# Optimization experiments

Measured on AMD Instinct MI355X. Metric: run time of the kernel, lower is better.

## Reference

```python
import jax, jax.numpy as jnp
import numpy as np
import math

S = 3  # num_subset

def _pe(C, T, V, domain):
    # sinusoidal positional encoding over flattened (T,V) grid -> [1,C,T,V]
    if domain == 'spatial':
        pos = np.tile(np.arange(V), T).astype(np.float32)
    else:
        pos = np.repeat(np.arange(T), V).astype(np.float32)
    div = np.exp(np.arange(0, C, 2).astype(np.float32) * (-math.log(10000.0) / C))
    pe = np.zeros((T * V, C), np.float32)
    pe[:, 0::2] = np.sin(pos[:, None] * div)
    pe[:, 1::2] = np.cos(pos[:, None] * div)
    return jnp.asarray(pe.reshape(T, V, C).transpose(2, 0, 1)[None])

def _conv1(x, W, b):  # 1x1 Conv2d == per-pixel channel matmul
    return jnp.einsum('oc,nctv->notv', W, x) + b[None, :, None, None]

def _bn(x, p):  # eval-mode BatchNorm2d; p: [4,C] = gamma, beta, run_mean, run_var
    g, b, m, v = p
    inv = g / jnp.sqrt(v + 1e-5)
    return (x - m[:, None, None]) * inv[:, None, None] + b[:, None, None]

def _lrelu(x):
    return jnp.where(x > 0, x, 0.1 * x)  # LeakyReLU(0.1)

def _forward(x, Wqk_s, bqk_s, alphas, att0s, Wo_s, bo_s, bn_o_s, Wf_s, bf_s, bn_f_s,
             Wqk_t, bqk_t, alphat, att0t, Wo_t, bo_t, bn_o_t, Wf_t, bf_t, bn_f_t):
    N, C, T, V = x.shape
    R = Wqk_s.shape[0] // (2 * S)  # inter_channels
    # ---- spatial attention (atts buffer is zeros; downs are identity since in==out, stride=1) ----
    y = x + _pe(C, T, V, 'spatial')
    qk = _conv1(y, Wqk_s, bqk_s).reshape(N, 2 * S, R, T, V)
    q, k = qk[:, :S], qk[:, S:]
    att = jnp.tanh(jnp.einsum('nsctu,nsctv->nsuv', q, k) / (R * T)) * alphas + att0s
    y = jnp.einsum('nctu,nsuv->nsctv', x, att).reshape(N, S * C, T, V)
    y = _lrelu(x + _bn(_conv1(y, Wo_s, bo_s), bn_o_s))      # out_nets + residual
    y = _lrelu(x + _bn(_conv1(y, Wf_s, bf_s), bn_f_s))      # ff_nets  + residual
    # ---- temporal attention (attt buffer is zeros; downt are identity) ----
    z = y + _pe(C, T, V, 'temporal')
    qk = _conv1(z, Wqk_t, bqk_t).reshape(N, 2 * S, R, T, V)
    q, k = qk[:, :S], qk[:, S:]
    att = jnp.tanh(jnp.einsum('nsctv,nscqv->nstq', q, k) / (R * V)) * alphat + att0t
    z = jnp.einsum('nctv,nstq->nscqv', y, att).reshape(N, S * C, T, V)
    z = _lrelu(y + _bn(_conv1(z, Wo_t, bo_t), bn_o_t))      # out_nett + residual
    z = _lrelu(y + _bn(_conv1(z, Wf_t, bf_t), bn_f_t))      # ff_nett  + residual
    return z

def setup_inputs() -> dict:
    key = jax.random.key(0)
    ks = jax.random.split(key, 12)
    N, C, T, V, R = 128, 128, 64, 25, 32
    def w(k, o, i):
        return jax.random.normal(k, (o, i), jnp.float32) * np.float32(np.sqrt(2.0 / i))
    def bnp(k, c):
        k1, k2, k3 = jax.random.split(k, 3)
        return jnp.stack([1.0 + 0.1 * jax.random.normal(k1, (c,)),
                          0.1 * jax.random.normal(k2, (c,)),
                          0.1 * jax.random.normal(k3, (c,)),
                          jnp.ones((c,))])
    return {
        'x': jax.random.normal(ks[0], (N, C, T, V), jnp.float32),
        'Wqk_s': w(ks[1], 2 * S * R, C), 'bqk_s': jnp.zeros((2 * S * R,), jnp.float32),
        'alphas': jnp.ones((1, S, 1, 1), jnp.float32),
        'att0s': jnp.ones((1, S, V, V), jnp.float32) / V,
        'Wo_s': w(ks[2], C, S * C), 'bo_s': jnp.zeros((C,), jnp.float32), 'bn_o_s': bnp(ks[3], C),
        'Wf_s': w(ks[4], C, C), 'bf_s': jnp.zeros((C,), jnp.float32), 'bn_f_s': bnp(ks[5], C),
        'Wqk_t': w(ks[6], 2 * S * R, C), 'bqk_t': jnp.zeros((2 * S * R,), jnp.float32),
        'alphat': jnp.ones((1, S, 1, 1), jnp.float32),
        'att0t': jnp.broadcast_to(jnp.eye(T, dtype=jnp.float32), (1, S, T, T)).copy(),
        'Wo_t': w(ks[7], C, S * C), 'bo_t': jnp.zeros((C,), jnp.float32), 'bn_o_t': bnp(ks[8], C),
        'Wf_t': w(ks[9], C, C), 'bf_t': jnp.zeros((C,), jnp.float32), 'bn_f_t': bnp(ks[10], C),
    }

def reference(x, Wqk_s, bqk_s, alphas, att0s, Wo_s, bo_s, bn_o_s, Wf_s, bf_s, bn_f_s,
              Wqk_t, bqk_t, alphat, att0t, Wo_t, bo_t, bn_o_t, Wf_t, bf_t, bn_f_t):
    return _forward(x, Wqk_s, bqk_s, alphas, att0s, Wo_s, bo_s, bn_o_s, Wf_s, bf_s, bn_f_s,
                    Wqk_t, bqk_t, alphat, att0t, Wo_t, bo_t, bn_o_t, Wf_t, bf_t, bn_f_t)
```

## Files before the change

kernel.cpp:

```cpp
#include <hip/hip_runtime.h>
#include <math.h>


typedef __attribute__((ext_vector_type(8))) short short8v;
typedef __attribute__((ext_vector_type(4))) float f32x4;

__device__ __forceinline__ ushort f2bf(float f) {
    uint b = __float_as_uint(f);
    uint r = b + 0x7fffu + ((b >> 16) & 1u);
    return (ushort)(r >> 16);
}
__device__ __forceinline__ float bf2f(ushort h) {
    return __uint_as_float(((uint)h) << 16);
}

__global__ __launch_bounds__(256) void wt_prep(
    const float* __restrict__ Wo_s, const float* __restrict__ Wf_s,
    const float* __restrict__ Wo_t, const float* __restrict__ Wf_t,
    const float* __restrict__ Wqk_s, const float* __restrict__ Wqk_t,
    ushort* __restrict__ W16)
{
    int idx = blockIdx.x * 256 + threadIdx.x;
    if (idx >= 180224) return;
    float v;
    if (idx < 49152) {
        int s = idx / 16384, rem = idx % 16384, o = rem / 128, c = rem % 128;
        v = Wo_s[o * 384 + s * 128 + c];
    } else if (idx < 65536) {
        v = Wf_s[idx - 49152];
    } else if (idx < 114688) {
        int i = idx - 65536, s = i / 16384, rem = i % 16384, o = rem / 128, c = rem % 128;
        v = Wo_t[o * 384 + s * 128 + c];
    } else if (idx < 131072) {
        v = Wf_t[idx - 114688];
    } else if (idx < 155648) {
        v = Wqk_s[idx - 131072];
    } else {
        v = Wqk_t[idx - 155648];
    }
    W16[idx] = f2bf(v);
}

__global__ __launch_bounds__(256) void qk_pe_mfma(
    const float* __restrict__ src, const ushort* __restrict__ Wbf,
    const float* __restrict__ bias, ushort* __restrict__ out, int pos_is_t)
{
    __shared__ __align__(16) ushort xT[160 * 136];
    __shared__ __align__(16) ushort exch[192 * 24];
    const int n = blockIdx.y, tvb = blockIdx.x * 160;
    const float* sn = src + (size_t)n * 204800;
    for (int i = threadIdx.x; i < 2560; i += 256) {
        int tv4 = (i & 7) + (i >> 9) * 8;
        int cp  = (i >> 3) & 63;
        float4 a = *(const float4*)(sn + (2 * cp) * 1600 + tvb + tv4 * 4);
        float4 b = *(const float4*)(sn + (2 * cp + 1) * 1600 + tvb + tv4 * 4);
        float dv = __expf(-0.14391156831212787f * (float)cp);
        float av[4] = { a.x, a.y, a.z, a.w };
        float bv[4] = { b.x, b.y, b.z, b.w };
#pragma unroll
        for (int e = 0; e < 4; e++) {
            int tv = tvb + tv4 * 4 + e;
            int tt = tv / 25;
            float pos = pos_is_t ? (float)tt : (float)(tv - tt * 25);
            float ang = pos * dv;
            uint p = (uint)f2bf(av[e] + __sinf(ang)) | ((uint)f2bf(bv[e] + __cosf(ang)) << 16);
            ((uint*)xT)[(tv4 * 4 + e) * 68 + cp] = p;
        }
    }
    __syncthreads();
    const int lane = threadIdx.x & 63, wave = threadIdx.x >> 6;
    const int l15 = lane & 15, kg = lane >> 4;
    const int rb = wave * 48;
    short8v wf[3][4];
#pragma unroll
    for (int nt = 0; nt < 3; nt++)
#pragma unroll
        for (int k = 0; k < 4; k++)
            wf[nt][k] = *(const short8v*)&Wbf[(rb + nt * 16 + l15) * 128 + k * 32 + kg * 8];
    float bsv[3];
#pragma unroll
    for (int nt = 0; nt < 3; nt++) bsv[nt] = bias[rb + nt * 16 + l15];
    ushort* on = out + (size_t)n * 307200;
    for (int mt = 0; mt < 10; mt++) {
        short8v af[4];
#pragma unroll
        for (int k = 0; k < 4; k++)
            af[k] = *(short8v*)&xT[(mt * 16 + l15) * 136 + k * 32 + kg * 8];
        f32x4 accs[3];
#pragma unroll
        for (int nt = 0; nt < 3; nt++) {
            f32x4 acc = {0.f, 0.f, 0.f, 0.f};
#pragma unroll
            for (int k = 0; k < 4; k++)
                acc = __builtin_amdgcn_mfma_f32_16x16x32_bf16(af[k], wf[nt][k], acc, 0, 0, 0);
            accs[nt] = acc;
        }
        __syncthreads();
#pragma unroll
        for (int nt = 0; nt < 3; nt++) {
            uint2 pk;
            pk.x = (uint)f2bf(accs[nt][0] + bsv[nt]) | ((uint)f2bf(accs[nt][1] + bsv[nt]) << 16);
            pk.y = (uint)f2bf(accs[nt][2] + bsv[nt]) | ((uint)f2bf(accs[nt][3] + bsv[nt]) << 16);
            *(uint2*)&exch[(rb + nt * 16 + l15) * 24 + kg * 4] = pk;
        }
        __syncthreads();
        for (int i = threadIdx.x; i < 384; i += 256) {
            int r = i >> 1, hh = i & 1;
            *(uint4*)(on + (size_t)r * 1600 + tvb + mt * 16 + hh * 8) =
                *(const uint4*)&exch[r * 24 + hh * 8];
        }
    }
}

__global__ __launch_bounds__(256) void att_s_mfma(
    const ushort* __restrict__ qk, const float* __restrict__ alphas,
    const float* __restrict__ att0, ushort* __restrict__ attS_bf)
{
    __shared__ __align__(16) ushort Qs[32 * 520];
    __shared__ __align__(16) ushort Ks[32 * 520];
    const int s = blockIdx.x, n = blockIdx.y;
    const ushort* qb = qk + (size_t)n * 307200 + (size_t)(s * 32) * 1600;
    const ushort* kb = qb + 96 * 1600;
    for (int i = threadIdx.x; i < 3072; i += 256) {
        int v = i / 96, k = i - v * 96;
        if (v >= 25 || (k & 31) >= 25) attS_bf[(size_t)n * 3072 + i] = 0;
    }
    const int lane = threadIdx.x & 63, wave = threadIdx.x >> 6;
    const int l15 = lane & 15, kg = lane >> 4;
    const int mt = wave >> 1, nt = wave & 1;
    f32x4 acc = {0.f, 0.f, 0.f, 0.f};
    for (int rc = 0; rc < 4; rc++) {
        __syncthreads();
        for (int i = threadIdx.x; i < 6400; i += 256) {
            int rl = i / 800, j = i - rl * 800;
            uint uq = *(const uint*)(qb + (rc * 8 + rl) * 1600 + j * 2);
            uint uk = *(const uint*)(kb + (rc * 8 + rl) * 1600 + j * 2);
            int tv = j * 2;
            int t0 = tv / 25, u0 = tv - t0 * 25;
            int t1 = (tv + 1) / 25, u1 = (tv + 1) - t1 * 25;
            Qs[u0 * 520 + rl * 64 + t0] = (ushort)(uq & 0xffffu);
            Qs[u1 * 520 + rl * 64 + t1] = (ushort)(uq >> 16);
            Ks[u0 * 520 + rl * 64 + t0] = (ushort)(uk & 0xffffu);
            Ks[u1 * 520 + rl * 64 + t1] = (ushort)(uk >> 16);
        }
        __syncthreads();
#pragma unroll
        for (int ks = 0; ks < 16; ks++) {
            short8v a = *(const short8v*)&Qs[(mt * 16 + l15) * 520 + ks * 32 + kg * 8];
            short8v b = *(const short8v*)&Ks[(nt * 16 + l15) * 520 + ks * 32 + kg * 8];
            acc = __builtin_amdgcn_mfma_f32_16x16x32_bf16(a, b, acc, 0, 0, 0);
        }
    }
    float alpha = alphas[s];
#pragma unroll
    for (int rr = 0; rr < 4; rr++) {
        int u = mt * 16 + kg * 4 + rr, v = nt * 16 + l15;
        if (u < 25 && v < 25)
            attS_bf[(size_t)n * 3072 + v * 96 + s * 32 + u] =
                f2bf(tanhf(acc[rr] * (1.0f / 2048.0f)) * alpha + att0[s * 625 + u * 25 + v]);
    }
}

__global__ __launch_bounds__(256) void att_t_mfma(
    const ushort* __restrict__ qk, const float* __restrict__ alphat,
    const float* __restrict__ att0, ushort* __restrict__ attT_bf)
{
    __shared__ __align__(16) ushort Qt[8 * 64 * 40];
    __shared__ __align__(16) ushort Kt[8 * 64 * 40];
    const int s = blockIdx.x, n = blockIdx.y;
    const ushort* qb = qk + (size_t)n * 307200 + (size_t)(s * 32) * 1600;
    const ushort* kb = qb + 96 * 1600;
    for (int i = threadIdx.x; i < 10240; i += 256) {
        ((uint*)Qt)[i] = 0u;
        ((uint*)Kt)[i] = 0u;
    }
    const int lane = threadIdx.x & 63, wave = threadIdx.x >> 6;
    const int l15 = lane & 15, kg = lane >> 4;
    const int mt = wave;
    f32x4 acc[4];
#pragma unroll
    for (int i = 0; i < 4; i++) acc[i] = (f32x4){0.f, 0.f, 0.f, 0.f};
    for (int rc = 0; rc < 4; rc++) {
        __syncthreads();
        for (int i = threadIdx.x; i < 6400; i += 256) {
            int rl = i / 800, j = i - rl * 800;
            uint uq = *(const uint*)(qb + (rc * 8 + rl) * 1600 + j * 2);
            uint uk = *(const uint*)(kb + (rc * 8 + rl) * 1600 + j * 2);
            int tv = j * 2;
            int t0 = tv / 25, v0 = tv - t0 * 25;
            int t1 = (tv + 1) / 25, v1 = (tv + 1) - t1 * 25;
            Qt[(rl * 64 + t0) * 40 + v0] = (ushort)(uq & 0xffffu);
            Qt[(rl * 64 + t1) * 40 + v1] = (ushort)(uq >> 16);
            Kt[(rl * 64 + t0) * 40 + v0] = (ushort)(uk & 0xffffu);
            Kt[(rl * 64 + t1) * 40 + v1] = (ushort)(uk >> 16);
        }
        __syncthreads();
#pragma unroll
        for (int rl = 0; rl < 8; rl++) {
            short8v a = *(const short8v*)&Qt[(rl * 64 + mt * 16 + l15) * 40 + kg * 8];
#pragma unroll
            for (int nq = 0; nq < 4; nq++) {
                short8v b = *(const short8v*)&Kt[(rl * 64 + nq * 16 + l15) * 40 + kg * 8];
                acc[nq] = __builtin_amdgcn_mfma_f32_16x16x32_bf16(a, b, acc[nq], 0, 0, 0);
            }
        }
    }
    float alpha = alphat[s];
#pragma unroll
    for (int nq = 0; nq < 4; nq++) {
        int q = nq * 16 + l15;
        ushort w4[4];
#pragma unroll
        for (int rr = 0; rr < 4; rr++) {
            int t = mt * 16 + kg * 4 + rr;
            w4[rr] = f2bf(tanhf(acc[nq][rr] * (1.0f / 800.0f)) * alpha +
                          att0[s * 4096 + t * 64 + q]);
        }
        uint2 pk;
        pk.x = (uint)w4[0] | ((uint)w4[1] << 16);
        pk.y = (uint)w4[2] | ((uint)w4[3] << 16);
        *(uint2*)(attT_bf + (size_t)n * 12288 + q * 192 + s * 64 + mt * 16 + kg * 4) = pk;
    }
}

__global__ __launch_bounds__(256) void s_fused(
    const float* __restrict__ x, const ushort* __restrict__ Wo ,
    const ushort* __restrict__ attS , const ushort* __restrict__ Wf,
    const float* __restrict__ bnO, const float* __restrict__ boO,
    const float* __restrict__ bnF, const float* __restrict__ bfF,
    float* __restrict__ outp)
{
    __shared__ __align__(16) ushort xT[64 * 136];
    __shared__ __align__(16) ushort Bt[256 * 32];
    __shared__ __align__(16) ushort y1T[64 * 136];
    __shared__ float sc1[128], of1[128], sc2[128], of2[128];
    const int n = blockIdx.y, tb = blockIdx.x;
    const int tvg0 = tb * 50;
    if (threadIdx.x < 128) {
        int o = threadIdx.x;
        float s1 = bnO[o] * rsqrtf(bnO[384 + o] + 1e-5f);
        sc1[o] = s1; of1[o] = (boO[o] - bnO[256 + o]) * s1 + bnO[128 + o];
    } else {
        int o = threadIdx.x - 128;
        float s2 = bnF[o] * rsqrtf(bnF[384 + o] + 1e-5f);
        sc2[o] = s2; of2[o] = (bfF[o] - bnF[256 + o]) * s2 + bnF[128 + o];
    }
    for (int i = threadIdx.x; i < 1792; i += 256) {
        int nr = i / 7, k = 25 + i % 7;
        Bt[nr * 32 + (((k >> 3) ^ ((nr >> 1) & 3)) << 3) + (k & 7)] = 0;
    }
    const float* xn = x + (size_t)n * 204800;
    for (int i = threadIdx.x; i < 3200; i += 256) {
        int c = i / 25, j2 = i - c * 25;
        float2 v2 = *(const float2*)(xn + c * 1600 + tvg0 + j2 * 2);
        xT[(j2 * 2) * 136 + c]     = f2bf(v2.x);
        xT[(j2 * 2 + 1) * 136 + c] = f2bf(v2.y);
    }
    __syncthreads();
    const int lane = threadIdx.x & 63, wave = threadIdx.x >> 6;
    const int l15 = lane & 15, kg = lane >> 4;
    const int ob = wave * 32, jb = wave * 4;
    f32x4 accS[2][4];
#pragma unroll
    for (int mt = 0; mt < 2; mt++)
#pragma unroll
        for (int jj = 0; jj < 4; jj++) accS[mt][jj] = (f32x4){0.f, 0.f, 0.f, 0.f};
    const ushort* An = attS + (size_t)n * 3072;
    for (int s = 0; s < 3; s++) {
        short8v bW[2][4];
#pragma unroll
        for (int ot = 0; ot < 2; ot++)
#pragma unroll
            for (int k = 0; k < 4; k++)
                bW[ot][k] = *(const short8v*)&Wo[s * 16384 +
                             (ob + ot * 16 + l15) * 128 + k * 32 + kg * 8];
#pragma unroll
        for (int tt = 0; tt < 4; tt++) {
            short8v aX[4];
#pragma unroll
            for (int k = 0; k < 4; k++)
                aX[k] = *(short8v*)&xT[(tt * 16 + l15) * 136 + k * 32 + kg * 8];
            f32x4 h0 = {0.f, 0.f, 0.f, 0.f}, h1 = {0.f, 0.f, 0.f, 0.f};
#pragma unroll
            for (int k = 0; k < 4; k++) {
                h0 = __builtin_amdgcn_mfma_f32_16x16x32_bf16(aX[k], bW[0][k], h0, 0, 0, 0);
                h1 = __builtin_amdgcn_mfma_f32_16x16x32_bf16(aX[k], bW[1][k], h1, 0, 0, 0);
            }
#pragma unroll
            for (int rr = 0; rr < 4; rr++) {
                int tv = tt * 16 + kg * 4 + rr;
                if (tv < 50) {
                    int tl = tv >= 25 ? 1 : 0, u = tv - tl * 25;
                    int n0 = tl * 128 + ob + l15;
                    int n1 = n0 + 16;
                    Bt[n0 * 32 + (((u >> 3) ^ ((n0 >> 1) & 3)) << 3) + (u & 7)] = f2bf(h0[rr]);
                    Bt[n1 * 32 + (((u >> 3) ^ ((n1 >> 1) & 3)) << 3) + (u & 7)] = f2bf(h1[rr]);
                }
            }
        }
        __syncthreads();
        short8v aA[2];
#pragma unroll
        for (int mt = 0; mt < 2; mt++)
            aA[mt] = *(const short8v*)(An + (mt * 16 + l15) * 96 + s * 32 + kg * 8);
#pragma unroll
        for (int jj = 0; jj < 4; jj++) {
            int nr = (jb + jj) * 16 + l15;
            short8v b = *(const short8v*)&Bt[nr * 32 + ((kg ^ ((nr >> 1) & 3)) << 3)];
#pragma unroll
            for (int mt = 0; mt < 2; mt++)
                accS[mt][jj] = __builtin_amdgcn_mfma_f32_16x16x32_bf16(aA[mt], b, accS[mt][jj], 0, 0, 0);
        }
        __syncthreads();
    }
#pragma unroll
    for (int mt = 0; mt < 2; mt++)
#pragma unroll
        for (int jj = 0; jj < 4; jj++) {
            int nr = (jb + jj) * 16 + l15;
            int tl = nr >> 7, o = nr & 127;
            float sc = sc1[o], of = of1[o];
#pragma unroll
            for (int rr = 0; rr < 4; rr++) {
                int v = mt * 16 + kg * 4 + rr;
                if (v < 25) {
                    int tvl = tl * 25 + v;
                    float h = accS[mt][jj][rr] * sc + of + bf2f(xT[tvl * 136 + o]);
                    h = h > 0.f ? h : 0.1f * h;
                    y1T[tvl * 136 + o] = f2bf(h);
                }
            }
        }
    __syncthreads();
    short8v aF[2][4];
#pragma unroll
    for (int mt = 0; mt < 2; mt++)
#pragma unroll
        for (int k = 0; k < 4; k++)
            aF[mt][k] = *(const short8v*)&Wf[(ob + mt * 16 + l15) * 128 + k * 32 + kg * 8];
    float* on = outp + (size_t)n * 204800;
#pragma unroll
    for (int nt = 0; nt < 4; nt++) {
        short8v bY[4];
#pragma unroll
        for (int k = 0; k < 4; k++)
            bY[k] = *(short8v*)&y1T[(nt * 16 + l15) * 136 + k * 32 + kg * 8];
        f32x4 c0 = {0.f, 0.f, 0.f, 0.f}, c1 = {0.f, 0.f, 0.f, 0.f};
#pragma unroll
        for (int k = 0; k < 4; k++) {
            c0 = __builtin_amdgcn_mfma_f32_16x16x32_bf16(aF[0][k], bY[k], c0, 0, 0, 0);
            c1 = __builtin_amdgcn_mfma_f32_16x16x32_bf16(aF[1][k], bY[k], c1, 0, 0, 0);
        }
        int tv = nt * 16 + l15;
        if (tv < 50) {
#pragma unroll
            for (int rr = 0; rr < 4; rr++) {
                {
                    int o = ob + kg * 4 + rr;
                    float h = c0[rr] * sc2[o] + of2[o] + bf2f(xT[tv * 136 + o]);
                    on[(size_t)o * 1600 + tvg0 + tv] = h > 0.f ? h : 0.1f * h;
                }
                {
                    int o = ob + 16 + kg * 4 + rr;
                    float h = c1[rr] * sc2[o] + of2[o] + bf2f(xT[tv * 136 + o]);
                    on[(size_t)o * 1600 + tvg0 + tv] = h > 0.f ? h : 0.1f * h;
                }
            }
        }
    }
}

__global__ __launch_bounds__(256) void y_cvt(
    const float* __restrict__ y, ushort* __restrict__ y_bf)
{
    __shared__ __align__(16) ushort xT[160 * 136];
    const int np = blockIdx.y, tvb = blockIdx.x * 160;
    const float* sn = y + (size_t)np * 204800;
    for (int i = threadIdx.x; i < 2560; i += 256) {
        int tv4 = (i & 7) + (i >> 9) * 8;
        int cp  = (i >> 3) & 63;
        float4 a = *(const float4*)(sn + (2 * cp) * 1600 + tvb + tv4 * 4);
        float4 b = *(const float4*)(sn + (2 * cp + 1) * 1600 + tvb + tv4 * 4);
        float av[4] = { a.x, a.y, a.z, a.w };
        float bv[4] = { b.x, b.y, b.z, b.w };
#pragma unroll
        for (int e = 0; e < 4; e++) {
            uint p = (uint)f2bf(av[e]) | ((uint)f2bf(bv[e]) << 16);
            ((uint*)xT)[(tv4 * 4 + e) * 68 + cp] = p;
        }
    }
    __syncthreads();
    uint* dst = (uint*)(y_bf + (size_t)np * 204800 + (size_t)tvb * 128);
    for (int i = threadIdx.x; i < 10240; i += 256) {
        int tv = i >> 6, cp = i & 63;
        dst[tv * 64 + cp] = ((const uint*)xT)[tv * 68 + cp];
    }
}

__global__ __launch_bounds__(256) void tt_fused(
    ushort* __restrict__ ybuf ,
    const ushort* __restrict__ Wo ,
    const ushort* __restrict__ attT ,
    const float* __restrict__ bnp, const float* __restrict__ bo)
{
    __shared__ __align__(16) ushort yS[64 * 136];
    __shared__ __align__(16) ushort Gl[128 * 72];
    __shared__ float sc_l[128], of_l[128];
    const int v = blockIdx.x, np = blockIdx.y;
    if (threadIdx.x < 128) {
        int o = threadIdx.x;
        float sc = bnp[o] * rsqrtf(bnp[384 + o] + 1e-5f);
        sc_l[o] = sc;
        of_l[o] = (bo[o] - bnp[256 + o]) * sc + bnp[128 + o];
    }
    ushort* yq = ybuf + (size_t)np * 204800;
    for (int i = threadIdx.x; i < 4096; i += 256) {
        int t = i >> 6, cp = i & 63;
        ((uint*)yS)[t * 68 + cp] = *(const uint*)(yq + (size_t)(t * 25 + v) * 128 + cp * 2);
    }
    __syncthreads();
    const int lane = threadIdx.x & 63, wave = threadIdx.x >> 6;
    const int l15 = lane & 15, kg = lane >> 4;
    const int ob = wave * 32;
    const ushort* An = attT + (size_t)np * 12288;
    f32x4 acc[4][2];
#pragma unroll
    for (int mt = 0; mt < 4; mt++)
#pragma unroll
        for (int jj = 0; jj < 2; jj++) acc[mt][jj] = (f32x4){0.f, 0.f, 0.f, 0.f};
    for (int s = 0; s < 3; s++) {
        short8v bW[2][4];
#pragma unroll
        for (int nt = 0; nt < 2; nt++)
#pragma unroll
            for (int k = 0; k < 4; k++)
                bW[nt][k] = *(const short8v*)&Wo[s * 16384 +
                             (ob + nt * 16 + l15) * 128 + k * 32 + kg * 8];
#pragma unroll
        for (int mt = 0; mt < 4; mt++) {
            short8v aX[4];
#pragma unroll
            for (int k = 0; k < 4; k++)
                aX[k] = *(short8v*)&yS[(mt * 16 + l15) * 136 + k * 32 + kg * 8];
            f32x4 g0 = {0.f, 0.f, 0.f, 0.f}, g1 = {0.f, 0.f, 0.f, 0.f};
#pragma unroll
            for (int k = 0; k < 4; k++) {
                g0 = __builtin_amdgcn_mfma_f32_16x16x32_bf16(aX[k], bW[0][k], g0, 0, 0, 0);
                g1 = __builtin_amdgcn_mfma_f32_16x16x32_bf16(aX[k], bW[1][k], g1, 0, 0, 0);
            }
#pragma unroll
            for (int rr = 0; rr < 4; rr++) {
                int t = mt * 16 + kg * 4 + rr;
                Gl[(ob + l15) * 72 + t]      = f2bf(g0[rr]);
                Gl[(ob + 16 + l15) * 72 + t] = f2bf(g1[rr]);
            }
        }
        __syncthreads();
#pragma unroll
        for (int ks = 0; ks < 2; ks++) {
            short8v b2[2];
#pragma unroll
            for (int jj = 0; jj < 2; jj++)
                b2[jj] = *(short8v*)&Gl[(ob + jj * 16 + l15) * 72 + ks * 32 + kg * 8];
#pragma unroll
            for (int mt = 0; mt < 4; mt++) {
                short8v a2 = *(const short8v*)(An + (mt * 16 + l15) * 192 + s * 64 + ks * 32 + kg * 8);
#pragma unroll
                for (int jj = 0; jj < 2; jj++)
                    acc[mt][jj] = __builtin_amdgcn_mfma_f32_16x16x32_bf16(a2, b2[jj], acc[mt][jj], 0, 0, 0);
            }
        }
        __syncthreads();
    }
#pragma unroll
    for (int mt = 0; mt < 4; mt++)
#pragma unroll
        for (int jj = 0; jj < 2; jj++) {
            int o = ob + jj * 16 + l15;
            float sc = sc_l[o], of = of_l[o];
#pragma unroll
            for (int rr = 0; rr < 4; rr++) {
                int q = mt * 16 + kg * 4 + rr;
                float h = acc[mt][jj][rr] * sc + of + bf2f(yS[q * 136 + o]);
                h = h > 0.f ? h : 0.1f * h;
                yq[(size_t)(q * 25 + v) * 128 + o] = f2bf(h);
            }
        }
}

__global__ __launch_bounds__(256) void cbr_mfma(
    const ushort* __restrict__ y1 , const float* res,
    const ushort* __restrict__ Wbf, const float* __restrict__ bias,
    const float* __restrict__ bnp, float* outp)
{
    __shared__ __align__(16) ushort xT[160 * 136];
    __shared__ float sc_l[128], of_l[128];
    const int np = blockIdx.y, tvb = blockIdx.x * 160;
    if (threadIdx.x < 128) {
        int o = threadIdx.x;
        float sc = bnp[o] * rsqrtf(bnp[384 + o] + 1e-5f);
        sc_l[o] = sc;
        of_l[o] = (bias[o] - bnp[256 + o]) * sc + bnp[128 + o];
    }
    const ushort* pp = y1 + (size_t)np * 204800 + (size_t)tvb * 128;
    for (int i = threadIdx.x; i < 10240; i += 256) {
        int tl = i >> 6, cp = i & 63;
        ((uint*)xT)[tl * 68 + cp] = *(const uint*)(pp + tl * 128 + cp * 2);
    }
    __syncthreads();
    const int lane = threadIdx.x & 63, wave = threadIdx.x >> 6;
    const int l15 = lane & 15, kg = lane >> 4;
    const int ob = wave * 32;
    short8v af[2][4];
#pragma unroll
    for (int mt = 0; mt < 2; mt++)
#pragma unroll
        for (int k = 0; k < 4; k++)
            af[mt][k] = *(const short8v*)&Wbf[(ob + mt * 16 + l15) * 128 + k * 32 + kg * 8];
    const float* res_n = res + (size_t)np * 204800;
    float* out_n = outp + (size_t)np * 204800;
    for (int nt = 0; nt < 10; nt++) {
        short8v bfg[4];
#pragma unroll
        for (int k = 0; k < 4; k++)
            bfg[k] = *(short8v*)&xT[(nt * 16 + l15) * 136 + k * 32 + kg * 8];
        f32x4 acc0 = {0.f, 0.f, 0.f, 0.f};
        f32x4 acc1 = {0.f, 0.f, 0.f, 0.f};
#pragma unroll
        for (int k = 0; k < 4; k++) {
            acc0 = __builtin_amdgcn_mfma_f32_16x16x32_bf16(af[0][k], bfg[k], acc0, 0, 0, 0);
            acc1 = __builtin_amdgcn_mfma_f32_16x16x32_bf16(af[1][k], bfg[k], acc1, 0, 0, 0);
        }
        int tv = tvb + nt * 16 + l15;
#pragma unroll
        for (int rr = 0; rr < 4; rr++) {
            {
                int o = ob + kg * 4 + rr;
                size_t idx = (size_t)o * 1600 + tv;
                float h = acc0[rr] * sc_l[o] + of_l[o] + res_n[idx];
                out_n[idx] = h > 0.f ? h : 0.1f * h;
            }
            {
                int o = ob + 16 + kg * 4 + rr;
                size_t idx = (size_t)o * 1600 + tv;
                float h = acc1[rr] * sc_l[o] + of_l[o] + res_n[idx];
                out_n[idx] = h > 0.f ? h : 0.1f * h;
            }
        }
    }
}

extern "C" void kernel_launch(void* const* d_in, const int* in_sizes, int n_in,
                              void* d_out, int out_size, void* d_ws, size_t ws_size,
                              hipStream_t stream)
{
    (void)in_sizes; (void)n_in; (void)out_size; (void)ws_size;
    const float* x      = (const float*)d_in[0];
    const float* Wqk_s  = (const float*)d_in[1];
    const float* bqk_s  = (const float*)d_in[2];
    const float* alphas = (const float*)d_in[3];
    const float* att0s  = (const float*)d_in[4];
    const float* Wo_s   = (const float*)d_in[5];
    const float* bo_s   = (const float*)d_in[6];
    const float* bn_o_s = (const float*)d_in[7];
    const float* Wf_s   = (const float*)d_in[8];
    const float* bf_s   = (const float*)d_in[9];
    const float* bn_f_s = (const float*)d_in[10];
    const float* Wqk_t  = (const float*)d_in[11];
    const float* bqk_t  = (const float*)d_in[12];
    const float* alphat = (const float*)d_in[13];
    const float* att0t  = (const float*)d_in[14];
    const float* Wo_t   = (const float*)d_in[15];
    const float* bo_t   = (const float*)d_in[16];
    const float* bn_o_t = (const float*)d_in[17];
    const float* Wf_t   = (const float*)d_in[18];
    const float* bf_t   = (const float*)d_in[19];
    const float* bn_f_t = (const float*)d_in[20];

    float* out = (float*)d_out;
    ushort* qk      = (ushort*)d_ws;
    ushort* ybuf    = (ushort*)d_ws;
    ushort* attS_bf = (ushort*)((char*)d_ws + 78643200);
    ushort* attT_bf = (ushort*)((char*)d_ws + 79603200);
    ushort* W16     = (ushort*)((char*)d_ws + 85894656);
    const ushort* WoS_bf  = W16;
    const ushort* WfS_bf  = W16 + 49152;
    const ushort* WoT_bf  = W16 + 65536;
    const ushort* WfT_bf  = W16 + 114688;
    const ushort* WqkS_bf = W16 + 131072;
    const ushort* WqkT_bf = W16 + 155648;

    wt_prep<<<704, 256, 0, stream>>>(Wo_s, Wf_s, Wo_t, Wf_t, Wqk_s, Wqk_t, W16);

    dim3 gqk(10, 128), gatt(3, 128), gsf(32, 128), gyc(10, 128), gtt(25, 128), gcbr(10, 128);

    qk_pe_mfma<<<gqk, 256, 0, stream>>>(x, WqkS_bf, bqk_s, qk, 0);
    att_s_mfma<<<gatt, 256, 0, stream>>>(qk, alphas, att0s, attS_bf);
    s_fused<<<gsf, 256, 0, stream>>>(x, WoS_bf, attS_bf, WfS_bf,
                                     bn_o_s, bo_s, bn_f_s, bf_s, out);

    qk_pe_mfma<<<gqk, 256, 0, stream>>>(out, WqkT_bf, bqk_t, qk, 1);
    att_t_mfma<<<gatt, 256, 0, stream>>>(qk, alphat, att0t, attT_bf);
    y_cvt<<<gyc, 256, 0, stream>>>(out, ybuf);
    tt_fused<<<gtt, 256, 0, stream>>>(ybuf, WoT_bf, attT_bf, bn_o_t, bo_t);
    cbr_mfma<<<gcbr, 256, 0, stream>>>(ybuf, out, WfT_bf, bf_t, bn_f_t, out);
}
```

Before: 506.3 us.

## Fuse temporal FF conv into t_fused and keep intermediate y in bf16 token-major

The spatial block now writes its output directly as bf16 in token-major layout instead of fp32 channel-major, which removes the y_cvt conversion kernel. A new qk_pe_bf kernel reads that bf16 buffer for the temporal QK projection. The temporal out-conv and feed-forward conv are merged into one t_fused kernel, so the separate cbr_mfma pass and its fp32 residual reread go away. The qk scratch buffer is moved into the output buffer. In exchange, the residual y is now held in bf16, which lowers precision, and t_fused writes its fp32 output with strided stores.

Measured after the change: 571.2 us. +12.8%, slower.

```diff
diff --git a/kernel.cpp b/kernel.cpp
--- a/kernel.cpp
+++ b/kernel.cpp
@@ -43,7 +43,7 @@
 
 __global__ __launch_bounds__(256) void qk_pe_mfma(
     const float* __restrict__ src, const ushort* __restrict__ Wbf,
-    const float* __restrict__ bias, ushort* __restrict__ out, int pos_is_t)
+    const float* __restrict__ bias, ushort* __restrict__ out)
 {
     __shared__ __align__(16) ushort xT[160 * 136];
     __shared__ __align__(16) ushort exch[192 * 24];
@@ -61,11 +61,74 @@
         for (int e = 0; e < 4; e++) {
             int tv = tvb + tv4 * 4 + e;
             int tt = tv / 25;
-            float pos = pos_is_t ? (float)tt : (float)(tv - tt * 25);
+            float pos = (float)(tv - tt * 25);
             float ang = pos * dv;
             uint p = (uint)f2bf(av[e] + __sinf(ang)) | ((uint)f2bf(bv[e] + __cosf(ang)) << 16);
             ((uint*)xT)[(tv4 * 4 + e) * 68 + cp] = p;
         }
+    }
+    __syncthreads();
+    const int lane = threadIdx.x & 63, wave = threadIdx.x >> 6;
+    const int l15 = lane & 15, kg = lane >> 4;
+    const int rb = wave * 48;
+    short8v wf[3][4];
+#pragma unroll
+    for (int nt = 0; nt < 3; nt++)
+#pragma unroll
+        for (int k = 0; k < 4; k++)
+            wf[nt][k] = *(const short8v*)&Wbf[(rb + nt * 16 + l15) * 128 + k * 32 + kg * 8];
+    float bsv[3];
+#pragma unroll
+    for (int nt = 0; nt < 3; nt++) bsv[nt] = bias[rb + nt * 16 + l15];
+    ushort* on = out + (size_t)n * 307200;
+    for (int mt = 0; mt < 10; mt++) {
+        short8v af[4];
+#pragma unroll
+        for (int k = 0; k < 4; k++)
+            af[k] = *(short8v*)&xT[(mt * 16 + l15) * 136 + k * 32 + kg * 8];
+        f32x4 accs[3];
+#pragma unroll
+        for (int nt = 0; nt < 3; nt++) {
+            f32x4 acc = {0.f, 0.f, 0.f, 0.f};
+#pragma unroll
+            for (int k = 0; k < 4; k++)
+                acc = __builtin_amdgcn_mfma_f32_16x16x32_bf16(af[k], wf[nt][k], acc, 0, 0, 0);
+            accs[nt] = acc;
+        }
+        __syncthreads();
+#pragma unroll
+        for (int nt = 0; nt < 3; nt++) {
+            uint2 pk;
+            pk.x = (uint)f2bf(accs[nt][0] + bsv[nt]) | ((uint)f2bf(accs[nt][1] + bsv[nt]) << 16);
+            pk.y = (uint)f2bf(accs[nt][2] + bsv[nt]) | ((uint)f2bf(accs[nt][3] + bsv[nt]) << 16);
+            *(uint2*)&exch[(rb + nt * 16 + l15) * 24 + kg * 4] = pk;
+        }
+        __syncthreads();
+        for (int i = threadIdx.x; i < 384; i += 256) {
+            int r = i >> 1, hh = i & 1;
+            *(uint4*)(on + (size_t)r * 1600 + tvb + mt * 16 + hh * 8) =
+                *(const uint4*)&exch[r * 24 + hh * 8];
+        }
+    }
+}
+
+__global__ __launch_bounds__(256) void qk_pe_bf(
+    const ushort* __restrict__ ybf, const ushort* __restrict__ Wbf,
+    const float* __restrict__ bias, ushort* __restrict__ out)
+{
+    __shared__ __align__(16) ushort xT[160 * 136];
+    __shared__ __align__(16) ushort exch[192 * 24];
+    const int n = blockIdx.y, tvb = blockIdx.x * 160;
+    const ushort* yq = ybf + (size_t)n * 204800;
+    for (int i = threadIdx.x; i < 10240; i += 256) {
+        int tv = i >> 6, cp = i & 63;
+        uint w = *(const uint*)(yq + (size_t)(tvb + tv) * 128 + cp * 2);
+        int t = (tvb + tv) / 25;
+        float dv = __expf(-0.14391156831212787f * (float)cp);
+        float ang = (float)t * dv;
+        float lo = bf2f((ushort)(w & 0xffffu)) + __sinf(ang);
+        float hi = bf2f((ushort)(w >> 16)) + __cosf(ang);
+        ((uint*)xT)[tv * 68 + cp] = (uint)f2bf(lo) | ((uint)f2bf(hi) << 16);
     }
     __syncthreads();
     const int lane = threadIdx.x & 63, wave = threadIdx.x >> 6;
@@ -228,11 +291,10 @@
     const ushort* __restrict__ attS , const ushort* __restrict__ Wf,
     const float* __restrict__ bnO, const float* __restrict__ boO,
     const float* __restrict__ bnF, const float* __restrict__ bfF,
-    float* __restrict__ outp)
+    ushort* __restrict__ ybf)
 {
     __shared__ __align__(16) ushort xT[64 * 136];
-    __shared__ __align__(16) ushort Bt[256 * 32];
-    __shared__ __align__(16) ushort y1T[64 * 136];
+    __shared__ __align__(16) ushort uni[64 * 136];
     __shared__ float sc1[128], of1[128], sc2[128], of2[128];
     const int n = blockIdx.y, tb = blockIdx.x;
     const int tvg0 = tb * 50;
@@ -245,6 +307,7 @@
         float s2 = bnF[o] * rsqrtf(bnF[384 + o] + 1e-5f);
         sc2[o] = s2; of2[o] = (bfF[o] - bnF[256 + o]) * s2 + bnF[128 + o];
     }
+    ushort* Bt = uni;
     for (int i = threadIdx.x; i < 1792; i += 256) {
         int nr = i / 7, k = 25 + i % 7;
         Bt[nr * 32 + (((k >> 3) ^ ((nr >> 1) & 3)) << 3) + (k & 7)] = 0;
@@ -327,7 +390,7 @@
                     int tvl = tl * 25 + v;
                     float h = accS[mt][jj][rr] * sc + of + bf2f(xT[tvl * 136 + o]);
                     h = h > 0.f ? h : 0.1f * h;
-                    y1T[tvl * 136 + o] = f2bf(h);
+                    uni[tvl * 136 + o] = f2bf(h);
                 }
             }
         }
@@ -338,82 +401,71 @@
 #pragma unroll
         for (int k = 0; k < 4; k++)
             aF[mt][k] = *(const short8v*)&Wf[(ob + mt * 16 + l15) * 128 + k * 32 + kg * 8];
-    float* on = outp + (size_t)n * 204800;
+    f32x4 c0s[4], c1s[4];
 #pragma unroll
     for (int nt = 0; nt < 4; nt++) {
         short8v bY[4];
 #pragma unroll
         for (int k = 0; k < 4; k++)
-            bY[k] = *(short8v*)&y1T[(nt * 16 + l15) * 136 + k * 32 + kg * 8];
+            bY[k] = *(short8v*)&uni[(nt * 16 + l15) * 136 + k * 32 + kg * 8];
         f32x4 c0 = {0.f, 0.f, 0.f, 0.f}, c1 = {0.f, 0.f, 0.f, 0.f};
 #pragma unroll
         for (int k = 0; k < 4; k++) {
             c0 = __builtin_amdgcn_mfma_f32_16x16x32_bf16(aF[0][k], bY[k], c0, 0, 0, 0);
             c1 = __builtin_amdgcn_mfma_f32_16x16x32_bf16(aF[1][k], bY[k], c1, 0, 0, 0);
         }
+        c0s[nt] = c0; c1s[nt] = c1;
+    }
+    __syncthreads();
+#pragma unroll
+    for (int nt = 0; nt < 4; nt++) {
         int tv = nt * 16 + l15;
-        if (tv < 50) {
-#pragma unroll
-            for (int rr = 0; rr < 4; rr++) {
-                {
-                    int o = ob + kg * 4 + rr;
-                    float h = c0[rr] * sc2[o] + of2[o] + bf2f(xT[tv * 136 + o]);
-                    on[(size_t)o * 1600 + tvg0 + tv] = h > 0.f ? h : 0.1f * h;
-                }
-                {
-                    int o = ob + 16 + kg * 4 + rr;
-                    float h = c1[rr] * sc2[o] + of2[o] + bf2f(xT[tv * 136 + o]);
-                    on[(size_t)o * 1600 + tvg0 + tv] = h > 0.f ? h : 0.1f * h;
-                }
-            }
-        }
-    }
-}
-
-__global__ __launch_bounds__(256) void y_cvt(
-    const float* __restrict__ y, ushort* __restrict__ y_bf)
-{
-    __shared__ __align__(16) ushort xT[160 * 136];
-    const int np = blockIdx.y, tvb = blockIdx.x * 160;
-    const float* sn = y + (size_t)np * 204800;
-    for (int i = threadIdx.x; i < 2560; i += 256) {
-        int tv4 = (i & 7) + (i >> 9) * 8;
-        int cp  = (i >> 3) & 63;
-        float4 a = *(const float4*)(sn + (2 * cp) * 1600 + tvb + tv4 * 4);
-        float4 b = *(const float4*)(sn + (2 * cp + 1) * 1600 + tvb + tv4 * 4);
-        float av[4] = { a.x, a.y, a.z, a.w };
-        float bv[4] = { b.x, b.y, b.z, b.w };
-#pragma unroll
-        for (int e = 0; e < 4; e++) {
-            uint p = (uint)f2bf(av[e]) | ((uint)f2bf(bv[e]) << 16);
-            ((uint*)xT)[(tv4 * 4 + e) * 68 + cp] = p;
-        }
-    }
-    __syncthreads();
-    uint* dst = (uint*)(y_bf + (size_t)np * 204800 + (size_t)tvb * 128);
-    for (int i = threadIdx.x; i < 10240; i += 256) {
+#pragma unroll
+        for (int rr = 0; rr < 4; rr++) {
+            {
+                int o = ob + kg * 4 + rr;
+                float h = c0s[nt][rr] * sc2[o] + of2[o] + bf2f(xT[tv * 136 + o]);
+                uni[tv * 136 + o] = f2bf(h > 0.f ? h : 0.1f * h);
+            }
+            {
+                int o = ob + 16 + kg * 4 + rr;
+                float h = c1s[nt][rr] * sc2[o] + of2[o] + bf2f(xT[tv * 136 + o]);
+                uni[tv * 136 + o] = f2bf(h > 0.f ? h : 0.1f * h);
+            }
+        }
+    }
+    __syncthreads();
+    uint* dst = (uint*)(ybf + (size_t)n * 204800 + (size_t)tvg0 * 128);
+    for (int i = threadIdx.x; i < 3200; i += 256) {
         int tv = i >> 6, cp = i & 63;
-        dst[tv * 64 + cp] = ((const uint*)xT)[tv * 68 + cp];
-    }
-}
-
-__global__ __launch_bounds__(256) void tt_fused(
-    ushort* __restrict__ ybuf ,
-    const ushort* __restrict__ Wo ,
+        dst[tv * 64 + cp] = ((const uint*)uni)[tv * 68 + cp];
+    }
+}
+
+__global__ __launch_bounds__(256) void t_fused(
+    const ushort* __restrict__ ybf, const ushort* __restrict__ Wo ,
+    const ushort* __restrict__ Wf ,
     const ushort* __restrict__ attT ,
-    const float* __restrict__ bnp, const float* __restrict__ bo)
+    const float* __restrict__ bn1, const float* __restrict__ bo1,
+    const float* __restrict__ bn2, const float* __restrict__ bf2v,
+    float* __restrict__ outp)
 {
     __shared__ __align__(16) ushort yS[64 * 136];
-    __shared__ __align__(16) ushort Gl[128 * 72];
-    __shared__ float sc_l[128], of_l[128];
+    __shared__ __align__(16) ushort uni[128 * 72];
+    __shared__ float sc1[128], of1[128], sc2[128], of2[128];
     const int v = blockIdx.x, np = blockIdx.y;
     if (threadIdx.x < 128) {
         int o = threadIdx.x;
-        float sc = bnp[o] * rsqrtf(bnp[384 + o] + 1e-5f);
-        sc_l[o] = sc;
-        of_l[o] = (bo[o] - bnp[256 + o]) * sc + bnp[128 + o];
-    }
-    ushort* yq = ybuf + (size_t)np * 204800;
+        float sc = bn1[o] * rsqrtf(bn1[384 + o] + 1e-5f);
+        sc1[o] = sc;
+        of1[o] = (bo1[o] - bn1[256 + o]) * sc + bn1[128 + o];
+    } else {
+        int o = threadIdx.x - 128;
+        float sc = bn2[o] * rsqrtf(bn2[384 + o] + 1e-5f);
+        sc2[o] = sc;
+        of2[o] = (bf2v[o] - bn2[256 + o]) * sc + bn2[128 + o];
+    }
+    const ushort* yq = ybf + (size_t)np * 204800;
     for (int i = threadIdx.x; i < 4096; i += 256) {
         int t = i >> 6, cp = i & 63;
         ((uint*)yS)[t * 68 + cp] = *(const uint*)(yq + (size_t)(t * 25 + v) * 128 + cp * 2);
@@ -423,6 +475,7 @@
     const int l15 = lane & 15, kg = lane >> 4;
     const int ob = wave * 32;
     const ushort* An = attT + (size_t)np * 12288;
+    ushort* Gl = uni;
     f32x4 acc[4][2];
 #pragma unroll
     for (int mt = 0; mt < 4; mt++)
@@ -477,74 +530,47 @@
 #pragma unroll
         for (int jj = 0; jj < 2; jj++) {
             int o = ob + jj * 16 + l15;
-            float sc = sc_l[o], of = of_l[o];
+            float sc = sc1[o], of = of1[o];
 #pragma unroll
             for (int rr = 0; rr < 4; rr++) {
                 int q = mt * 16 + kg * 4 + rr;
                 float h = acc[mt][jj][rr] * sc + of + bf2f(yS[q * 136 + o]);
                 h = h > 0.f ? h : 0.1f * h;
-                yq[(size_t)(q * 25 + v) * 128 + o] = f2bf(h);
-            }
-        }
-}
-
-__global__ __launch_bounds__(256) void cbr_mfma(
-    const ushort* __restrict__ y1 , const float* res,
-    const ushort* __restrict__ Wbf, const float* __restrict__ bias,
-    const float* __restrict__ bnp, float* outp)
-{
-    __shared__ __align__(16) ushort xT[160 * 136];
-    __shared__ float sc_l[128], of_l[128];
-    const int np = blockIdx.y, tvb = blockIdx.x * 160;
-    if (threadIdx.x < 128) {
-        int o = threadIdx.x;
-        float sc = bnp[o] * rsqrtf(bnp[384 + o] + 1e-5f);
-        sc_l[o] = sc;
-        of_l[o] = (bias[o] - bnp[256 + o]) * sc + bnp[128 + o];
-    }
-    const ushort* pp = y1 + (size_t)np * 204800 + (size_t)tvb * 128;
-    for (int i = threadIdx.x; i < 10240; i += 256) {
-        int tl = i >> 6, cp = i & 63;
-        ((uint*)xT)[tl * 68 + cp] = *(const uint*)(pp + tl * 128 + cp * 2);
-    }
-    __syncthreads();
-    const int lane = threadIdx.x & 63, wave = threadIdx.x >> 6;
-    const int l15 = lane & 15, kg = lane >> 4;
-    const int ob = wave * 32;
-    short8v af[2][4];
-#pragma unroll
-    for (int mt = 0; mt < 2; mt++)
-#pragma unroll
-        for (int k = 0; k < 4; k++)
-            af[mt][k] = *(const short8v*)&Wbf[(ob + mt * 16 + l15) * 128 + k * 32 + kg * 8];
-    const float* res_n = res + (size_t)np * 204800;
+                uni[q * 136 + o] = f2bf(h);
+            }
+        }
+    __syncthreads();
+    short8v aF[2][4];
+#pragma unroll
+    for (int ot = 0; ot < 2; ot++)
+#pragma unroll
+        for (int k = 0; k < 4; k++)
+            aF[ot][k] = *(const short8v*)&Wf[(ob + ot * 16 + l15) * 128 + k * 32 + kg * 8];
     float* out_n = outp + (size_t)np * 204800;
-    for (int nt = 0; nt < 10; nt++) {
-        short8v bfg[4];
-#pragma unroll
-        for (int k = 0; k < 4; k++)
-            bfg[k] = *(short8v*)&xT[(nt * 16 + l15) * 136 + k * 32 + kg * 8];
-        f32x4 acc0 = {0.f, 0.f, 0.f, 0.f};
-        f32x4 acc1 = {0.f, 0.f, 0.f, 0.f};
+#pragma unroll
+    for (int qt = 0; qt < 4; qt++) {
+        short8v bY[4];
+#pragma unroll
+        for (int k = 0; k < 4; k++)
+            bY[k] = *(short8v*)&uni[(qt * 16 + l15) * 136 + k * 32 + kg * 8];
+        f32x4 c0 = {0.f, 0.f, 0.f, 0.f}, c1 = {0.f, 0.f, 0.f, 0.f};
 #pragma unroll
         for (int k = 0; k < 4; k++) {
-            acc0 = __builtin_amdgcn_mfma_f32_16x16x32_bf16(af[0][k], bfg[k], acc0, 0, 0, 0);
-            acc1 = __builtin_amdgcn_mfma_f32_16x16x32_bf16(af[1][k], bfg[k], acc1, 0, 0, 0);
-        }
-        int tv = tvb + nt * 16 + l15;
+            c0 = __builtin_amdgcn_mfma_f32_16x16x32_bf16(aF[0][k], bY[k], c0, 0, 0, 0);
+            c1 = __builtin_amdgcn_mfma_f32_16x16x32_bf16(aF[1][k], bY[k], c1, 0, 0, 0);
+        }
+        int q = qt * 16 + l15;
 #pragma unroll
         for (int rr = 0; rr < 4; rr++) {
             {
                 int o = ob + kg * 4 + rr;
-                size_t idx = (size_t)o * 1600 + tv;
-                float h = acc0[rr] * sc_l[o] + of_l[o] + res_n[idx];
-                out_n[idx] = h > 0.f ? h : 0.1f * h;
+                float h = c0[rr] * sc2[o] + of2[o] + bf2f(yS[q * 136 + o]);
+                out_n[(size_t)o * 1600 + q * 25 + v] = h > 0.f ? h : 0.1f * h;
             }
             {
                 int o = ob + 16 + kg * 4 + rr;
-                size_t idx = (size_t)o * 1600 + tv;
-                float h = acc1[rr] * sc_l[o] + of_l[o] + res_n[idx];
-                out_n[idx] = h > 0.f ? h : 0.1f * h;
+                float h = c1[rr] * sc2[o] + of2[o] + bf2f(yS[q * 136 + o]);
+                out_n[(size_t)o * 1600 + q * 25 + v] = h > 0.f ? h : 0.1f * h;
             }
         }
     }
@@ -578,8 +604,8 @@
     const float* bn_f_t = (const float*)d_in[20];
 
     float* out = (float*)d_out;
-    ushort* qk      = (ushort*)d_ws;
-    ushort* ybuf    = (ushort*)d_ws;
+    ushort* qk_d    = (ushort*)d_out;
+    ushort* ybf     = (ushort*)d_ws;
     ushort* attS_bf = (ushort*)((char*)d_ws + 78643200);
     ushort* attT_bf = (ushort*)((char*)d_ws + 79603200);
     ushort* W16     = (ushort*)((char*)d_ws + 85894656);
@@ -592,16 +618,15 @@
 
     wt_prep<<<704, 256, 0, stream>>>(Wo_s, Wf_s, Wo_t, Wf_t, Wqk_s, Wqk_t, W16);
 
-    dim3 gqk(10, 128), gatt(3, 128), gsf(32, 128), gyc(10, 128), gtt(25, 128), gcbr(10, 128);
-
-    qk_pe_mfma<<<gqk, 256, 0, stream>>>(x, WqkS_bf, bqk_s, qk, 0);
-    att_s_mfma<<<gatt, 256, 0, stream>>>(qk, alphas, att0s, attS_bf);
+    dim3 gqk(10, 128), gatt(3, 128), gsf(32, 128), gtf(25, 128);
+
+    qk_pe_mfma<<<gqk, 256, 0, stream>>>(x, WqkS_bf, bqk_s, qk_d);
+    att_s_mfma<<<gatt, 256, 0, stream>>>(qk_d, alphas, att0s, attS_bf);
     s_fused<<<gsf, 256, 0, stream>>>(x, WoS_bf, attS_bf, WfS_bf,
-                                     bn_o_s, bo_s, bn_f_s, bf_s, out);
-
-    qk_pe_mfma<<<gqk, 256, 0, stream>>>(out, WqkT_bf, bqk_t, qk, 1);
-    att_t_mfma<<<gatt, 256, 0, stream>>>(qk, alphat, att0t, attT_bf);
-    y_cvt<<<gyc, 256, 0, stream>>>(out, ybuf);
-    tt_fused<<<gtt, 256, 0, stream>>>(ybuf, WoT_bf, attT_bf, bn_o_t, bo_t);
-    cbr_mfma<<<gcbr, 256, 0, stream>>>(ybuf, out, WfT_bf, bf_t, bn_f_t, out);
-}
+                                     bn_o_s, bo_s, bn_f_s, bf_s, ybf);
+
+    qk_pe_bf<<<gqk, 256, 0, stream>>>(ybf, WqkT_bf, bqk_t, qk_d);
+    att_t_mfma<<<gatt, 256, 0, stream>>>(qk_d, alphat, att0t, attT_bf);
+    t_fused<<<gtf, 256, 0, stream>>>(ybf, WoT_bf, WfT_bf, attT_bf,
+                                     bn_o_t, bo_t, bn_f_t, bf_t, out);
+}
```
